# Kernel optimization log

Measured on AMD Instinct MI355X. Metric: run time of the kernel, lower is better.

## Reference

```python
import jax, jax.numpy as jnp
import numpy as np

IN, OUT, HID = 64, 32, 256
B, T = 64, 256
NOISE_STD, TAU = 0.05, 0.2


def setup_inputs() -> dict:
    key = jax.random.key(0)
    ks = jax.random.split(key, 8)
    u = jax.random.normal(ks[0], (B, T, IN), dtype=jnp.float32)
    x0 = jax.random.normal(ks[1], (B, HID), dtype=jnp.float32)
    noise = jax.random.normal(ks[2], (T, B, HID), dtype=jnp.float32)
    w_hh_rnn = jax.random.normal(ks[3], (HID, HID), dtype=jnp.float32) * (0.1 / HID ** 0.5)
    w_hh_tbrnn = jax.random.normal(ks[4], (HID, HID, HID), dtype=jnp.float32) * (0.1 / HID)
    w_in_w = jax.random.normal(ks[5], (HID, IN), dtype=jnp.float32)
    w_in_b = jnp.zeros((HID,), dtype=jnp.float32)
    w_out_w = jax.random.normal(ks[6], (OUT, HID), dtype=jnp.float32) * 4.0
    w_out_b = jax.random.normal(ks[7], (OUT,), dtype=jnp.float32) * 0.0
    return {"u": u, "x0": x0, "noise": noise, "w_hh_rnn": w_hh_rnn,
            "w_hh_tbrnn": w_hh_tbrnn, "w_in_w": w_in_w, "w_in_b": w_in_b,
            "w_out_w": w_out_w, "w_out_b": w_out_b}


def reference(u, x0, noise, w_hh_rnn, w_hh_tbrnn, w_in_w, w_in_b, w_out_w, w_out_b):
    # mode='cont', form='rate', adv=False, nonlinearity=tanh, output_nonlinearity=tanh
    u_t_first = jnp.transpose(u, (1, 0, 2))  # [T, B, IN]

    def step(x, inp):
        u_t, n_t = inp
        r = jnp.tanh(x)                                   # rate form
        input_I = u_t @ w_in_w.T + w_in_b                 # [B, HID]
        hidden_W1 = r @ w_hh_rnn.T                        # [B, HID]
        # out[b,j] = sum_{i,k} r[b,i] * W[j,i,k] * r[b,k]
        hidden_W2 = jnp.einsum('bi,jik,bk->bj', r, w_hh_tbrnn, r)
        rec_x = hidden_W1 + hidden_W2 + input_I
        x_new = x + NOISE_STD * n_t + TAU * (-x + rec_x)  # cont mode
        return x_new, x_new

    x_final, traj = jax.lax.scan(step, x0, (u_t_first, noise))
    trajectories = jnp.transpose(traj, (1, 0, 2))         # [B, T, HID]
    output = jnp.tanh(trajectories) @ w_out_w.T + w_out_b  # [B, T, OUT]
    return output, x_final, trajectories
```

## Files before the change

### kernel.cpp

```cpp
#include <hip/hip_runtime.h>
#include <hip/hip_bf16.h>
#include <math.h>

#define HID 256
#define BSZ 64
#define TLEN 256
#define INW 64
#define OUTW 32
#define NOISE_STD 0.05f
#define TAU 0.2f

typedef __attribute__((ext_vector_type(8))) short short8;
typedef __attribute__((ext_vector_type(4))) float floatx4;
typedef unsigned long long u64;

__device__ __forceinline__ int ridx(int b, int k) {
    int P = ((b >> 2) & 7) ^ ((b & 3) << 1);
    return b * 256 + ((((k >> 3) ^ P) & 31) << 3) + (k & 7);
}

__global__ __launch_bounds__(256) void swizzle_kernel(const float* __restrict__ W,
                                                      __hip_bfloat16* __restrict__ Wsw) {
    int g = blockIdx.x * 256 + threadIdx.x;
    int l  = g & 63;
    int ni = (g >> 6) & 15;
    int kk = (g >> 10) & 7;
    int j  = g >> 13;
    int i  = ni * 16 + (l & 15);
    int k0 = kk * 32 + (l >> 4) * 8;
    const float* __restrict__ src = W + ((size_t)j * HID + i) * HID + k0;
    __hip_bfloat16* __restrict__ dst = Wsw + (size_t)g * 8;
#pragma unroll
    for (int e = 0; e < 8; ++e) dst[e] = __float2bfloat16(src[e]);
}

__global__ __launch_bounds__(256) void init_kernel(const float* __restrict__ x0,
                                                   u64* __restrict__ buf0) {
    int g = blockIdx.x;
    int k = threadIdx.x;
    u64 v = 0;
#pragma unroll
    for (int e = 0; e < 4; ++e) {
        __hip_bfloat16 h = __float2bfloat16(tanhf(x0[(4 * g + e) * HID + k]));
        v |= (u64)(*(unsigned short*)&h) << (16 * e);
    }
    buf0[g * 256 + k] = v;
}

__global__ __launch_bounds__(256) void pre_kernel(const float* __restrict__ u,
                                                  const float* __restrict__ w_in_w,
                                                  const float* __restrict__ w_in_b,
                                                  const float* __restrict__ noise,
                                                  float* __restrict__ pre) {
    __shared__ float ulds[BSZ][INW + 4];
    const int t = blockIdx.x;
    const int j = threadIdx.x;
    {
        int b = threadIdx.x >> 2, q = threadIdx.x & 3;
#pragma unroll
        for (int e = 0; e < 4; ++e) {
            float4 v = *(const float4*)(u + ((size_t)b * TLEN + t) * INW + q * 16 + e * 4);
            *(float4*)&ulds[b][q * 16 + e * 4] = v;
        }
    }
    float wreg[INW];
#pragma unroll
    for (int q = 0; q < INW / 4; ++q) {
        float4 v = *(const float4*)(w_in_w + (size_t)j * INW + q * 4);
        wreg[q * 4 + 0] = v.x; wreg[q * 4 + 1] = v.y;
        wreg[q * 4 + 2] = v.z; wreg[q * 4 + 3] = v.w;
    }
    float bias = w_in_b[j];
    __syncthreads();
    for (int b = 0; b < BSZ; ++b) {
        float s = bias;
#pragma unroll
        for (int in_ = 0; in_ < INW; ++in_) s = fmaf(ulds[b][in_], wreg[in_], s);
        float nz = noise[((size_t)t * BSZ + b) * HID + j];
        pre[((size_t)t * HID + j) * BSZ + b] = NOISE_STD * nz + TAU * s;
    }
}

__global__ __launch_bounds__(256, 1) void persist_kernel(
    const __hip_bfloat16* __restrict__ Wsw,
    const float* __restrict__ w_hh,
    const float* __restrict__ u,
    const float* __restrict__ w_in_w,
    const float* __restrict__ w_in_b,
    const float* __restrict__ noise,
    const float* __restrict__ x0,
    u64* __restrict__ buf0,
    u64* __restrict__ buf1,
    float* __restrict__ traj,
    float* __restrict__ trajWS,
    float* __restrict__ xfinal,
    int* __restrict__ ready,
    const float* __restrict__ pre,
    int use_pre, int use_tws) {
    __shared__ short rlds[16384];
    __shared__ float redw[256];
    __shared__ char lds_pad[57344];

    const int tid  = threadIdx.x;
    const int j    = blockIdx.x;
    const int w    = tid >> 6;
    const int lane = tid & 63;
    const int quad = lane >> 4;
    const int col  = lane & 15;

    if (j == 0x7fffffff) lds_pad[tid] = 0;

    short8 wreg[32];
    {
        const short* __restrict__ wsh = (const short*)Wsw;
#pragma unroll
        for (int kk = 0; kk < 8; ++kk)
#pragma unroll
            for (int nj = 0; nj < 4; ++nj)
                wreg[kk * 4 + nj] = *(const short8*)(wsh +
                    ((((size_t)j * 8 + kk) * 16 + (w * 4 + nj)) * 64 + lane) * 8);
    }
    float whh_reg[4];
#pragma unroll
    for (int nj = 0; nj < 4; ++nj)
        whh_reg[nj] = w_hh[j * HID + (w * 4 + nj) * 16 + col];

    float xb = 0.f;
    if (tid < BSZ) xb = x0[tid * HID + j];

#pragma unroll 1
    for (int t = 0; t < TLEN; ++t) {
        const u64* __restrict__ rcur = (t & 1) ? buf1 : buf0;
        u64* __restrict__ rnxt = (t & 1) ? buf0 : buf1;

        float extra = 0.f;
        if (tid < BSZ) {
            if (use_pre) {
                extra = pre[((size_t)t * HID + j) * BSZ + tid];
            } else {
                float isum = w_in_b[j];
                const float4* __restrict__ urow =
                    (const float4*)(u + ((size_t)tid * TLEN + t) * INW);
                const float4* __restrict__ wrow = (const float4*)(w_in_w + (size_t)j * INW);
#pragma unroll
                for (int q = 0; q < INW / 4; ++q) {
                    float4 uu = urow[q], ww = wrow[q];
                    isum = fmaf(uu.x, ww.x, isum);
                    isum = fmaf(uu.y, ww.y, isum);
                    isum = fmaf(uu.z, ww.z, isum);
                    isum = fmaf(uu.w, ww.w, isum);
                }
                float nz = noise[((size_t)t * BSZ + tid) * HID + j];
                extra = NOISE_STD * nz + TAU * isum;
            }
        }

        if (t > 0) {
            while (__hip_atomic_load(ready + tid * 16, __ATOMIC_RELAXED,
                                     __HIP_MEMORY_SCOPE_AGENT) < t)
                __builtin_amdgcn_s_sleep(1);
            asm volatile("" ::: "memory");
        }

        {
            u64 v[16];
#pragma unroll
            for (int g = 0; g < 16; ++g)
                v[g] = __hip_atomic_load(rcur + g * 256 + tid, __ATOMIC_RELAXED,
                                         __HIP_MEMORY_SCOPE_AGENT);
#pragma unroll
            for (int g = 0; g < 16; ++g)
#pragma unroll
                for (int e = 0; e < 4; ++e)
                    rlds[ridx(4 * g + e, tid)] = (short)(v[g] >> (16 * e));
        }
        __syncthreads();

        floatx4 acc[4][4];
#pragma unroll
        for (int mb = 0; mb < 4; ++mb)
#pragma unroll
            for (int nj = 0; nj < 4; ++nj) acc[mb][nj] = (floatx4){0.f, 0.f, 0.f, 0.f};

#pragma unroll
        for (int kk = 0; kk < 8; ++kk) {
            short8 afrag[4];
#pragma unroll
            for (int mb = 0; mb < 4; ++mb)
                afrag[mb] = *(const short8*)&rlds[ridx(mb * 16 + col, kk * 32 + quad * 8)];
#pragma unroll
            for (int nj = 0; nj < 4; ++nj)
#pragma unroll
                for (int mb = 0; mb < 4; ++mb)
                    acc[mb][nj] = __builtin_amdgcn_mfma_f32_16x16x32_bf16(
                        afrag[mb], wreg[kk * 4 + nj], acc[mb][nj], 0, 0, 0);
        }

        float part[16];
#pragma unroll
        for (int p = 0; p < 16; ++p) part[p] = 0.f;
#pragma unroll
        for (int nj = 0; nj < 4; ++nj) {
            int i = (w * 4 + nj) * 16 + col;
            float whh = whh_reg[nj];
#pragma unroll
            for (int mb = 0; mb < 4; ++mb)
#pragma unroll
                for (int reg = 0; reg < 4; ++reg) {
                    int b = mb * 16 + quad * 4 + reg;
                    short rs = rlds[ridx(b, i)];
                    float rv = __bfloat162float(*(__hip_bfloat16*)&rs);
                    part[mb * 4 + reg] = fmaf(rv, acc[mb][nj][reg] + whh, part[mb * 4 + reg]);
                }
        }
#pragma unroll
        for (int s = 1; s < 16; s <<= 1) {
#pragma unroll
            for (int p = 0; p < 16; ++p) part[p] += __shfl_xor(part[p], s, 64);
        }
        if (col == 0) {
#pragma unroll
            for (int mb = 0; mb < 4; ++mb)
#pragma unroll
                for (int reg = 0; reg < 4; ++reg)
                    redw[w * 64 + mb * 16 + quad * 4 + reg] = part[mb * 4 + reg];
        }
        __syncthreads();

        if (w == 0) {
            const int b = lane;
            float rec = redw[b] + redw[64 + b] + redw[128 + b] + redw[192 + b];
            float xn = xb + extra + TAU * (rec - xb);
            xb = xn;

            if (t < TLEN - 1) {
                __hip_bfloat16 h = __float2bfloat16(tanhf(xn));
                int hs = (int)(*(unsigned short*)&h);
                int src = 4 * (lane & 15);
                u64 pv = (u64)(unsigned)__shfl(hs, src + 0, 64)
                       | ((u64)(unsigned)__shfl(hs, src + 1, 64) << 16)
                       | ((u64)(unsigned)__shfl(hs, src + 2, 64) << 32)
                       | ((u64)(unsigned)__shfl(hs, src + 3, 64) << 48);
                if (lane < 16)
                    __hip_atomic_store(rnxt + (size_t)lane * 256 + j, pv,
                                       __ATOMIC_RELAXED, __HIP_MEMORY_SCOPE_AGENT);
                asm volatile("s_waitcnt vmcnt(0)" ::: "memory");
                if (lane == 0)
                    __hip_atomic_store(ready + j * 16, t + 1, __ATOMIC_RELAXED,
                                       __HIP_MEMORY_SCOPE_AGENT);
            }

            if (use_tws) {
                trajWS[((size_t)t * HID + j) * BSZ + b] = xn;
            } else {
                traj[((size_t)b * TLEN + t) * HID + j] = xn;
                if (t == TLEN - 1) xfinal[b * HID + j] = xn;
            }
        }
    }
}

__global__ __launch_bounds__(256) void fixup_kernel(
    const float* __restrict__ trajWS,
    const float* __restrict__ w_out_w,
    const float* __restrict__ w_out_b,
    float* __restrict__ traj,
    float* __restrict__ xfinal,
    float* __restrict__ out) {
    __shared__ float xv[BSZ * 257];
    __shared__ float wol[OUTW * 257];
    const int t = blockIdx.x, tid = threadIdx.x;

#pragma unroll
    for (int it = 0; it < 16; ++it) {
        int flat = it * 1024 + tid * 4;
        float4 v = *(const float4*)(trajWS + (size_t)t * 16384 + flat);
        int jj = flat >> 6, b = flat & 63;
        xv[(b + 0) * 257 + jj] = v.x;
        xv[(b + 1) * 257 + jj] = v.y;
        xv[(b + 2) * 257 + jj] = v.z;
        xv[(b + 3) * 257 + jj] = v.w;
    }
#pragma unroll
    for (int it = 0; it < 8; ++it) {
        int flat = it * 1024 + tid * 4;
        float4 v = *(const float4*)(w_out_w + flat);
        int o = flat >> 8, h = flat & 255;
        *(float4*)&wol[o * 257 + h] = v;
    }
    __syncthreads();

    for (int b = 0; b < BSZ; ++b)
        traj[((size_t)b * TLEN + t) * HID + tid] = xv[b * 257 + tid];
    if (t == TLEN - 1)
        for (int b = 0; b < BSZ; ++b)
            xfinal[b * HID + tid] = xv[b * 257 + tid];

    __syncthreads();
#pragma unroll
    for (int it = 0; it < 64; ++it)
        xv[it * 257 + tid] = tanhf(xv[it * 257 + tid]);
    __syncthreads();

    const int o = tid & 31;
    const float bias = w_out_b[o];
#pragma unroll 1
    for (int rep = 0; rep < 8; ++rep) {
        int b = rep * 8 + (tid >> 5);
        float s = bias;
#pragma unroll 8
        for (int h = 0; h < HID; ++h)
            s = fmaf(xv[b * 257 + h], wol[o * 257 + h], s);
        out[((size_t)b * TLEN + t) * OUTW + o] = s;
    }
}

__global__ __launch_bounds__(256) void output_kernel(
    const float* __restrict__ traj, const float* __restrict__ w_out_w,
    const float* __restrict__ w_out_b, float* __restrict__ out) {
    __shared__ float th[8][HID + 1];
    const int bt0 = blockIdx.x * 8;
    const int tid = threadIdx.x;
#pragma unroll
    for (int m = 0; m < 8; ++m) {
        int idx = m * 256 + tid;
        th[idx >> 8][idx & 255] = tanhf(traj[(size_t)bt0 * HID + idx]);
    }
    __syncthreads();
    const int row = tid >> 5, o = tid & 31;
    const float* __restrict__ wrow = w_out_w + (size_t)o * HID;
    float s = w_out_b[o];
#pragma unroll 8
    for (int h = 0; h < HID; ++h) s = fmaf(th[row][h], wrow[h], s);
    out[(size_t)(bt0 + row) * OUTW + o] = s;
}

extern "C" void kernel_launch(void* const* d_in, const int* in_sizes, int n_in,
                              void* d_out, int out_size, void* d_ws, size_t ws_size,
                              hipStream_t stream) {
    const float* u       = (const float*)d_in[0];
    const float* x0      = (const float*)d_in[1];
    const float* noise   = (const float*)d_in[2];
    const float* w_hh    = (const float*)d_in[3];
    const float* W       = (const float*)d_in[4];
    const float* w_in_w  = (const float*)d_in[5];
    const float* w_in_b  = (const float*)d_in[6];
    const float* w_out_w = (const float*)d_in[7];
    const float* w_out_b = (const float*)d_in[8];

    float* out    = (float*)d_out;
    float* xfinal = out + (size_t)BSZ * TLEN * OUTW;
    float* traj   = xfinal + (size_t)BSZ * HID;

    char* ws = (char*)d_ws;
    __hip_bfloat16* Wsw = (__hip_bfloat16*)ws;
    u64*   buf0 = (u64*)(ws + 33554432);
    u64*   buf1 = (u64*)(ws + 33587200);
    int*   rdy  = (int*)(ws + 33619968);
    float* tws  = (float*)(ws + 33636352);
    float* pre  = (float*)(ws + 50413568);
    const size_t NEED_TWS = 50413568ull;
    const size_t NEED_PRE = 67190784ull;
    const int use_tws = (ws_size >= NEED_TWS) ? 1 : 0;
    const int use_pre = (ws_size >= NEED_PRE) ? 1 : 0;

    hipMemsetAsync(rdy, 0, 16384, stream);
    swizzle_kernel<<<8192, 256, 0, stream>>>(W, Wsw);
    init_kernel<<<16, 256, 0, stream>>>(x0, buf0);
    if (use_pre)
        pre_kernel<<<TLEN, 256, 0, stream>>>(u, w_in_w, w_in_b, noise, pre);

    persist_kernel<<<256, 256, 0, stream>>>(
        Wsw, w_hh, u, w_in_w, w_in_b, noise, x0,
        buf0, buf1, traj, tws, xfinal, rdy, pre, use_pre, use_tws);

    if (use_tws)
        fixup_kernel<<<TLEN, 256, 0, stream>>>(tws, w_out_w, w_out_b, traj, xfinal, out);
    else
        output_kernel<<<(BSZ * TLEN) / 8, 256, 0, stream>>>(traj, w_out_w, w_out_b, out);
}
```

Before: 1.635 ms.

## Replace ready-flag barrier with sentinel-valued 4-slot ring buffer for state exchange

Replaces the per-step ready counter polling plus separate data load with a 4-slot ring of packed bf16 rate values, where each slot is pre-filled with an all-ones sentinel and consumers poll the data itself until no sentinel remains. This removes one round-trip (flag load then data load) and the producer-side second store per step, and slots are re-armed two steps ahead. The ring layout is transposed so each thread loads contiguous data and writes two 16-byte LDS vectors with a new swizzle, replacing scalar short stores. It relies on a bf16 pair pattern never equalling the sentinel and on the ordering of relaxed stores across workgroups.

Measured after the change: 2.269 ms. 38.7% more time.

```diff
diff --git a/kernel.cpp b/kernel.cpp
--- a/kernel.cpp
+++ b/kernel.cpp
@@ -9,14 +9,15 @@
 #define OUTW 32
 #define NOISE_STD 0.05f
 #define TAU 0.2f
+#define SENT 0xFFFFFFFFFFFFFFFFull
 
 typedef __attribute__((ext_vector_type(8))) short short8;
 typedef __attribute__((ext_vector_type(4))) float floatx4;
 typedef unsigned long long u64;
 
-__device__ __forceinline__ int ridx(int b, int k) {
-    int P = ((b >> 2) & 7) ^ ((b & 3) << 1);
-    return b * 256 + ((((k >> 3) ^ P) & 31) << 3) + (k & 7);
+__device__ __forceinline__ int ridx2(int b, int k) {
+    int S = ((b >> 2) & 7) ^ (b & 3) ^ (((b >> 3) & 1) << 2);
+    return b * 256 + ((((k >> 3) ^ S) & 31) << 3) + (k & 7);
 }
 
 __global__ __launch_bounds__(256) void swizzle_kernel(const float* __restrict__ W,
@@ -35,16 +36,16 @@
 }
 
 __global__ __launch_bounds__(256) void init_kernel(const float* __restrict__ x0,
-                                                   u64* __restrict__ buf0) {
+                                                   u64* __restrict__ ring0) {
     int g = blockIdx.x;
-    int k = threadIdx.x;
+    int j = threadIdx.x;
     u64 v = 0;
 #pragma unroll
     for (int e = 0; e < 4; ++e) {
-        __hip_bfloat16 h = __float2bfloat16(tanhf(x0[(4 * g + e) * HID + k]));
+        __hip_bfloat16 h = __float2bfloat16(tanhf(x0[(4 * g + e) * HID + j]));
         v |= (u64)(*(unsigned short*)&h) << (16 * e);
     }
-    buf0[g * 256 + k] = v;
+    ring0[j * 16 + g] = v;
 }
 
 __global__ __launch_bounds__(256) void pre_kernel(const float* __restrict__ u,
@@ -89,12 +90,10 @@
     const float* __restrict__ w_in_b,
     const float* __restrict__ noise,
     const float* __restrict__ x0,
-    u64* __restrict__ buf0,
-    u64* __restrict__ buf1,
+    u64* __restrict__ ring,
     float* __restrict__ traj,
     float* __restrict__ trajWS,
     float* __restrict__ xfinal,
-    int* __restrict__ ready,
     const float* __restrict__ pre,
     int use_pre, int use_tws) {
     __shared__ short rlds[16384];
@@ -107,6 +106,8 @@
     const int lane = tid & 63;
     const int quad = lane >> 4;
     const int col  = lane & 15;
+    const int g    = tid >> 4;
+    const int j4   = tid & 15;
 
     if (j == 0x7fffffff) lds_pad[tid] = 0;
 
@@ -130,8 +131,7 @@
 
 #pragma unroll 1
     for (int t = 0; t < TLEN; ++t) {
-        const u64* __restrict__ rcur = (t & 1) ? buf1 : buf0;
-        u64* __restrict__ rnxt = (t & 1) ? buf0 : buf1;
+        u64* __restrict__ slot = ring + (size_t)(t & 3) * 4096;
 
         float extra = 0.f;
         if (tid < BSZ) {
@@ -155,26 +155,47 @@
             }
         }
 
+        u64 v[16];
+#pragma unroll
+        for (int m = 0; m < 16; ++m)
+            v[m] = __hip_atomic_load(slot + (j4 * 16 + m) * 16 + g,
+                                     __ATOMIC_RELAXED, __HIP_MEMORY_SCOPE_AGENT);
         if (t > 0) {
-            while (__hip_atomic_load(ready + tid * 16, __ATOMIC_RELAXED,
-                                     __HIP_MEMORY_SCOPE_AGENT) < t)
+            int pend = 0;
+#pragma unroll
+            for (int m = 0; m < 16; ++m) pend |= (v[m] == SENT);
+            while (pend) {
                 __builtin_amdgcn_s_sleep(1);
-            asm volatile("" ::: "memory");
-        }
-
-        {
-            u64 v[16];
-#pragma unroll
-            for (int g = 0; g < 16; ++g)
-                v[g] = __hip_atomic_load(rcur + g * 256 + tid, __ATOMIC_RELAXED,
-                                         __HIP_MEMORY_SCOPE_AGENT);
-#pragma unroll
-            for (int g = 0; g < 16; ++g)
-#pragma unroll
-                for (int e = 0; e < 4; ++e)
-                    rlds[ridx(4 * g + e, tid)] = (short)(v[g] >> (16 * e));
+                pend = 0;
+#pragma unroll
+                for (int m = 0; m < 16; ++m)
+                    if (v[m] == SENT) {
+                        v[m] = __hip_atomic_load(slot + (j4 * 16 + m) * 16 + g,
+                                                 __ATOMIC_RELAXED, __HIP_MEMORY_SCOPE_AGENT);
+                        pend |= (v[m] == SENT);
+                    }
+            }
+        }
+
+#pragma unroll
+        for (int e = 0; e < 4; ++e) {
+            const int b = 4 * g + e;
+            const int S = ((b >> 2) & 7) ^ (b & 3) ^ (((b >> 3) & 1) << 2);
+            short8 lo, hi;
+#pragma unroll
+            for (int m = 0; m < 8; ++m) {
+                lo[m] = (short)(v[m]     >> (16 * e));
+                hi[m] = (short)(v[m + 8] >> (16 * e));
+            }
+            short* dst = &rlds[b * 256];
+            *(short8*)(dst + ((((2 * j4 + 0) ^ S) & 31) << 3)) = lo;
+            *(short8*)(dst + ((((2 * j4 + 1) ^ S) & 31) << 3)) = hi;
         }
         __syncthreads();
+
+        if (w == 0 && lane < 16)
+            __hip_atomic_store(ring + (size_t)((t + 2) & 3) * 4096 + j * 16 + lane,
+                               SENT, __ATOMIC_RELAXED, __HIP_MEMORY_SCOPE_AGENT);
 
         floatx4 acc[4][4];
 #pragma unroll
@@ -187,7 +208,7 @@
             short8 afrag[4];
 #pragma unroll
             for (int mb = 0; mb < 4; ++mb)
-                afrag[mb] = *(const short8*)&rlds[ridx(mb * 16 + col, kk * 32 + quad * 8)];
+                afrag[mb] = *(const short8*)&rlds[ridx2(mb * 16 + col, kk * 32 + quad * 8)];
 #pragma unroll
             for (int nj = 0; nj < 4; ++nj)
 #pragma unroll
@@ -208,7 +229,7 @@
 #pragma unroll
                 for (int reg = 0; reg < 4; ++reg) {
                     int b = mb * 16 + quad * 4 + reg;
-                    short rs = rlds[ridx(b, i)];
+                    short rs = rlds[ridx2(b, i)];
                     float rv = __bfloat162float(*(__hip_bfloat16*)&rs);
                     part[mb * 4 + reg] = fmaf(rv, acc[mb][nj][reg] + whh, part[mb * 4 + reg]);
                 }
@@ -241,13 +262,10 @@
                        | ((u64)(unsigned)__shfl(hs, src + 1, 64) << 16)
                        | ((u64)(unsigned)__shfl(hs, src + 2, 64) << 32)
                        | ((u64)(unsigned)__shfl(hs, src + 3, 64) << 48);
+                asm volatile("s_waitcnt vmcnt(0)" ::: "memory");
                 if (lane < 16)
-                    __hip_atomic_store(rnxt + (size_t)lane * 256 + j, pv,
-                                       __ATOMIC_RELAXED, __HIP_MEMORY_SCOPE_AGENT);
-                asm volatile("s_waitcnt vmcnt(0)" ::: "memory");
-                if (lane == 0)
-                    __hip_atomic_store(ready + j * 16, t + 1, __ATOMIC_RELAXED,
-                                       __HIP_MEMORY_SCOPE_AGENT);
+                    __hip_atomic_store(ring + (size_t)((t + 1) & 3) * 4096 + j * 16 + lane,
+                                       pv, __ATOMIC_RELAXED, __HIP_MEMORY_SCOPE_AGENT);
             }
 
             if (use_tws) {
@@ -354,25 +372,23 @@
 
     char* ws = (char*)d_ws;
     __hip_bfloat16* Wsw = (__hip_bfloat16*)ws;
-    u64*   buf0 = (u64*)(ws + 33554432);
-    u64*   buf1 = (u64*)(ws + 33587200);
-    int*   rdy  = (int*)(ws + 33619968);
-    float* tws  = (float*)(ws + 33636352);
-    float* pre  = (float*)(ws + 50413568);
-    const size_t NEED_TWS = 50413568ull;
-    const size_t NEED_PRE = 67190784ull;
+    u64*   ring = (u64*)(ws + 33554432);
+    float* tws  = (float*)(ws + 33685504);
+    float* pre  = (float*)(ws + 50462720);
+    const size_t NEED_TWS = 50462720ull;
+    const size_t NEED_PRE = 67239936ull;
     const int use_tws = (ws_size >= NEED_TWS) ? 1 : 0;
     const int use_pre = (ws_size >= NEED_PRE) ? 1 : 0;
 
-    hipMemsetAsync(rdy, 0, 16384, stream);
+    hipMemsetAsync((char*)ring + 32768, 0xFF, 98304, stream);
     swizzle_kernel<<<8192, 256, 0, stream>>>(W, Wsw);
-    init_kernel<<<16, 256, 0, stream>>>(x0, buf0);
+    init_kernel<<<16, 256, 0, stream>>>(x0, ring);
     if (use_pre)
         pre_kernel<<<TLEN, 256, 0, stream>>>(u, w_in_w, w_in_b, noise, pre);
 
     persist_kernel<<<256, 256, 0, stream>>>(
         Wsw, w_hh, u, w_in_w, w_in_b, noise, x0,
-        buf0, buf1, traj, tws, xfinal, rdy, pre, use_pre, use_tws);
+        ring, traj, tws, xfinal, pre, use_pre, use_tws);
 
     if (use_tws)
         fixup_kernel<<<TLEN, 256, 0, stream>>>(tws, w_out_w, w_out_b, traj, xfinal, out);
```
